# Kernel tuning notes

Hardware: AMD Instinct MI355X
Metric: run time of the kernel (lower is better)

The kernel has to match this reference:

```python
import jax, jax.numpy as jnp
import numpy as np

N_NODES = 100000
N_EDGES = 3200000


def setup_inputs() -> dict:
    key = jax.random.key(0)
    ks = jax.random.split(key, 12)
    x = jax.random.normal(ks[0], (N_NODES, 5), dtype=jnp.float32)
    edges = jax.random.randint(ks[1], (2, N_EDGES), 0, N_NODES)
    edge_attr = jax.random.normal(ks[2], (N_EDGES, 2), dtype=jnp.float32)
    detector_labels = jax.random.bernoulli(ks[3], 0.7, (N_NODES,))

    def init(k, shape, fan_in):
        return (jax.random.normal(k, shape, dtype=jnp.float32) / np.sqrt(fan_in)).astype(jnp.float32)

    W_gat = init(ks[4], (5, 16), 5)        # GATConv lin (shared src/dst)
    att_src = init(ks[5], (16,), 16)
    att_dst = init(ks[6], (16,), 16)
    W_edge = init(ks[7], (2, 16), 2)       # GATConv lin_edge
    att_edge = init(ks[8], (16,), 16)
    b_gat = jnp.zeros((16,), jnp.float32)
    W1 = init(ks[9], (34, 64), 34)
    b1 = jnp.zeros((64,), jnp.float32)
    W2 = init(ks[10], (64, 2), 64)
    b2 = jnp.zeros((2,), jnp.float32)
    return dict(x=x, edges=edges, edge_attr=edge_attr, detector_labels=detector_labels,
                W_gat=W_gat, att_src=att_src, att_dst=att_dst, W_edge=W_edge,
                att_edge=att_edge, b_gat=b_gat, W1=W1, b1=b1, W2=W2, b2=b2)


def reference(x, edges, edge_attr, detector_labels, W_gat, att_src, att_dst,
              W_edge, att_edge, b_gat, W1, b1, W2, b2):
    n_nodes = x.shape[0]
    src, dst = edges[0], edges[1]

    # --- GATConv(5 -> 16, heads=1, concat=False, edge_dim=2, no self loops) ---
    h = x @ W_gat                                        # [N, 16]
    a_src = h @ att_src                                  # [N]
    a_dst = h @ att_dst                                  # [N]
    a_edge = (edge_attr @ W_edge) @ att_edge             # [E]
    alpha = jax.nn.leaky_relu(a_src[src] + a_dst[dst] + a_edge, 0.2)
    # segmented softmax over incoming edges of each dst node
    seg_max = jax.ops.segment_max(alpha, dst, num_segments=n_nodes)
    ex = jnp.exp(alpha - seg_max[dst])
    denom = jax.ops.segment_sum(ex, dst, num_segments=n_nodes)
    a = ex / (denom[dst] + 1e-16)                        # [E]
    out = jax.ops.segment_sum(h[src] * a[:, None], dst, num_segments=n_nodes) + b_gat
    xh = jax.nn.relu(out)                                # [N, 16]

    # --- edge update: gather-concat-MLP ---
    feat = jnp.concatenate([xh[src], edge_attr, xh[dst]], axis=-1)   # [E, 34]
    ef = jax.nn.relu(feat @ W1 + b1) @ W2 + b2                       # [E, 2]

    # --- SplitSyndromes: keep edges whose both endpoints are detectors ---
    valid = detector_labels[src] & detector_labels[dst]
    idx = jnp.nonzero(valid)[0]        # eager (data-dependent size, not jitted)
    return edges[:, idx], jax.nn.sigmoid(ef[idx])
```

## Files before the change

### kernel.cpp

```cpp
#include <hip/hip_runtime.h>

#define NN 100000
#define NE 3200000
#define CH 8192
#define NCB ((NE + CH - 1) / CH)
#define ITER (CH / 256)
#define NBK ((NN + 63) >> 6)
#define CAP 2560

__global__ void kdetect(const unsigned char* __restrict__ lab8, int* __restrict__ flags) {
  __shared__ int tmp[256];
  int t = threadIdx.x;
  int s = 0;
  for (int i = t; i < 25000; i += 256) s += lab8[4 * i + 1];
  tmp[t] = s;
  __syncthreads();
  for (int d = 128; d > 0; d >>= 1) { if (t < d) tmp[t] += tmp[t + d]; __syncthreads(); }
  if (t == 0) flags[0] = (tmp[0] != 0) ? 1 : 0;
}

__global__ void klab(const void* __restrict__ lab, const int* __restrict__ flags,
                     int* __restrict__ labN) {
  int n = blockIdx.x * 256 + threadIdx.x;
  if (n >= NN) return;
  int v;
  if (flags[0]) v = ((const unsigned char*)lab)[n];
  else          v = ((const int*)lab)[n];
  labN[n] = (v != 0) ? 1 : 0;
}

__global__ void kc01(const float* __restrict__ We, const float* __restrict__ ae,
                     float* __restrict__ c01) {
  if (threadIdx.x == 0) {
    float c0 = 0.f, c1 = 0.f;
    for (int k = 0; k < 16; k++) { c0 += We[k] * ae[k]; c1 += We[16 + k] * ae[k]; }
    c01[0] = c0; c01[1] = c1;
  }
}

__global__ void knodeA(const float* __restrict__ x, const float* __restrict__ Wg,
                       const float* __restrict__ atts, const float* __restrict__ attd,
                       float* __restrict__ a_src, float* __restrict__ a_dst) {
  int n = blockIdx.x * 256 + threadIdx.x;
  if (n >= NN) return;
  float xi[5];
#pragma unroll
  for (int i = 0; i < 5; i++) xi[i] = x[n * 5 + i];
  float asum = 0.f, dsum = 0.f;
#pragma unroll
  for (int k = 0; k < 16; k++) {
    float acc = 0.f;
#pragma unroll
    for (int i = 0; i < 5; i++) acc += xi[i] * Wg[i * 16 + k];
    asum += acc * atts[k];
    dsum += acc * attd[k];
  }
  a_src[n] = asum; a_dst[n] = dsum;
}

__global__ __launch_bounds__(256) void khist(const int* __restrict__ src,
                                             const int* __restrict__ dst,
                                             const int* __restrict__ labN,
                                             int* __restrict__ blkcnt,
                                             int* __restrict__ cntc) {
  __shared__ int hist[NBK];
  __shared__ int vsum;
  int tid = threadIdx.x, b = blockIdx.x;
  for (int i = tid; i < NBK; i += 256) hist[i] = 0;
  if (tid == 0) vsum = 0;
  __syncthreads();
  int wsum = 0;
  for (int it = 0; it < ITER; ++it) {
    int e = b * CH + it * 256 + tid;
    int v = 0;
    if (e < NE) {
      int s = src[e], d = dst[e];
      atomicAdd(&hist[d >> 6], 1);
      v = labN[s] & labN[d];
    }
    unsigned long long m = __ballot(v != 0);
    wsum += __popcll(m);
  }
  if ((tid & 63) == 0) atomicAdd(&vsum, wsum);
  __syncthreads();
  for (int i = tid; i < NBK; i += 256) blkcnt[i * NCB + b] = hist[i];
  if (tid == 0) cntc[b] = vsum;
}

__global__ __launch_bounds__(256) void kscanb(int* __restrict__ blkcnt,
                                              int* __restrict__ total) {
  __shared__ int a[512];
  int row = blockIdx.x, t = threadIdx.x;
  int* p = blkcnt + row * NCB;
  int o0 = (t < NCB) ? p[t] : 0;
  int o1 = (t + 256 < NCB) ? p[t + 256] : 0;
  a[t] = o0; a[t + 256] = o1;
  __syncthreads();
  for (int d = 1; d < 512; d <<= 1) {
    int x0 = (t >= d) ? a[t - d] : 0;
    int x1 = (t + 256 >= d) ? a[t + 256 - d] : 0;
    __syncthreads();
    a[t] += x0; a[t + 256] += x1;
    __syncthreads();
  }
  if (t < NCB) p[t] = a[t] - o0;
  if (t + 256 < NCB) p[t + 256] = a[t + 256] - o1;
  if (t == 0) total[row] = a[NCB - 1];
}

__global__ void kscan(const int* __restrict__ cnt, int* __restrict__ off, int nb) {
  __shared__ int tmp[256];
  __shared__ int carry;
  int t = threadIdx.x;
  if (t == 0) carry = 0;
  __syncthreads();
  for (int base = 0; base < nb; base += 256) {
    int i = base + t;
    int v = (i < nb) ? cnt[i] : 0;
    tmp[t] = v;
    __syncthreads();
    for (int d = 1; d < 256; d <<= 1) {
      int add = (t >= d) ? tmp[t - d] : 0;
      __syncthreads();
      tmp[t] += add;
      __syncthreads();
    }
    if (i < nb) off[i] = carry + tmp[t] - v;
    __syncthreads();
    if (t == 0) carry += tmp[255];
    __syncthreads();
  }
  if (t == 0) off[nb] = carry;
}

__global__ __launch_bounds__(256) void kscat(
    const int* __restrict__ src, const int* __restrict__ dst,
    const float* __restrict__ eattr, const int* __restrict__ labN,
    const float* __restrict__ a_src, const float* __restrict__ a_dst,
    const float* __restrict__ c01, const int* __restrict__ bucket_base,
    const int* __restrict__ blkcnt, const int* __restrict__ offc,
    uint2* __restrict__ bins, float* __restrict__ out,
    float2* __restrict__ eat2, int NV) {
  __shared__ int cur[NBK];
  __shared__ int wc[4];
  __shared__ int lbase;
  int b = blockIdx.x, tid = threadIdx.x;
  for (int i = tid; i < NBK; i += 256) cur[i] = bucket_base[i] + blkcnt[i * NCB + b];
  if (tid == 0) lbase = offc[b];
  float c0 = c01[0], c1 = c01[1];
  __syncthreads();
  int lane = tid & 63, wid = tid >> 6;
  for (int it = 0; it < ITER; ++it) {
    int e = b * CH + it * 256 + tid;
    int v = 0, s = 0, d = 0;
    float2 ea;
    if (e < NE) {
      s = src[e]; d = dst[e];
      ea = ((const float2*)eattr)[e];
      float al = a_src[s] + a_dst[d] + ea.x * c0 + ea.y * c1;
      al = (al > 0.f) ? al : 0.2f * al;
      float exv = __expf(al);
      int pos = atomicAdd(&cur[d >> 6], 1);
      uint2 pl;
      pl.x = ((unsigned)s << 6) | (unsigned)(d & 63);
      pl.y = __float_as_uint(exv);
      bins[pos] = pl;
      v = labN[s] & labN[d];
    }
    unsigned long long m = __ballot(v != 0);
    if (lane == 0) wc[wid] = __popcll(m);
    __syncthreads();
    int pre = 0;
    for (int i = 0; i < wid; i++) pre += wc[i];
    pre += __popcll(m & ((1ull << lane) - 1ull));
    if (v) {
      int p = lbase + pre;
      if (p < NV) {
        out[p] = (float)s;
        out[NV + p] = (float)d;
        eat2[p] = ea;
      }
    }
    __syncthreads();
    if (tid == 0) lbase += wc[0] + wc[1] + wc[2] + wc[3];
  }
}

__global__ __launch_bounds__(512) void kagg(
    const uint2* __restrict__ bins, const int* __restrict__ bucket_base,
    const float* __restrict__ x, const float* __restrict__ Wg,
    const float* __restrict__ bg, float* __restrict__ xh) {
  __shared__ uint2 pay[CAP];
  __shared__ int cnt[64], inc[64], cur[64];
  __shared__ float sWg[80], sbg[16];
  int k = blockIdx.x, tid = threadIdx.x;
  if (tid < 80) sWg[tid] = Wg[tid];
  else if (tid < 96) sbg[tid - 80] = bg[tid - 80];
  int start = bucket_base[k], end = bucket_base[k + 1];
  int node0 = k << 6;
  int c = tid & 15, g = tid >> 4;
  __syncthreads();
  float w0 = sWg[c], w1 = sWg[16 + c], w2 = sWg[32 + c], w3 = sWg[48 + c], w4 = sWg[64 + c];
  float acc[2] = {0.f, 0.f}, den[2] = {0.f, 0.f};
  for (int cb = start; cb < end; cb += CAP) {
    int n = min(end - cb, CAP);
    if (tid < 64) cnt[tid] = 0;
    __syncthreads();
    uint2 st0, st1, st2, st3, st4;
    {
      int i;
      i = tid;          if (i < n) { st0 = bins[cb + i]; atomicAdd(&cnt[st0.x & 63], 1); }
      i = tid + 512;    if (i < n) { st1 = bins[cb + i]; atomicAdd(&cnt[st1.x & 63], 1); }
      i = tid + 1024;   if (i < n) { st2 = bins[cb + i]; atomicAdd(&cnt[st2.x & 63], 1); }
      i = tid + 1536;   if (i < n) { st3 = bins[cb + i]; atomicAdd(&cnt[st3.x & 63], 1); }
      i = tid + 2048;   if (i < n) { st4 = bins[cb + i]; atomicAdd(&cnt[st4.x & 63], 1); }
    }
    __syncthreads();
    if (tid < 64) inc[tid] = cnt[tid];
    __syncthreads();
    for (int d = 1; d < 64; d <<= 1) {
      int v = 0;
      if (tid >= d && tid < 64) v = inc[tid - d];
      __syncthreads();
      if (tid < 64) inc[tid] += v;
      __syncthreads();
    }
    if (tid < 64) cur[tid] = inc[tid] - cnt[tid];
    __syncthreads();
    {
      int i;
      i = tid;          if (i < n) pay[atomicAdd(&cur[st0.x & 63], 1)] = st0;
      i = tid + 512;    if (i < n) pay[atomicAdd(&cur[st1.x & 63], 1)] = st1;
      i = tid + 1024;   if (i < n) pay[atomicAdd(&cur[st2.x & 63], 1)] = st2;
      i = tid + 1536;   if (i < n) pay[atomicAdd(&cur[st3.x & 63], 1)] = st3;
      i = tid + 2048;   if (i < n) pay[atomicAdd(&cur[st4.x & 63], 1)] = st4;
    }
    __syncthreads();
#pragma unroll
    for (int p = 0; p < 2; ++p) {
      int nd = p * 32 + g;
      int re = inc[nd], rs = re - cnt[nd];
      float a = 0.f, ds = 0.f;
      for (int idx = rs; idx < re; ++idx) {
        uint2 pl = pay[idx];
        int s = (int)(pl.x >> 6);
        float exv = __uint_as_float(pl.y);
        const float* xp = x + s * 5;
        float h = xp[0] * w0 + xp[1] * w1 + xp[2] * w2 + xp[3] * w3 + xp[4] * w4;
        a += h * exv;
        ds += exv;
      }
      acc[p] += a; den[p] += ds;
    }
    __syncthreads();
  }
#pragma unroll
  for (int p = 0; p < 2; ++p) {
    int node = node0 + p * 32 + g;
    if (node < NN) {
      float dn = fmaxf(den[p], 1e-30f);
      float v = acc[p] / dn + sbg[c];
      xh[node * 16 + c] = (v > 0.f) ? v : 0.f;
    }
  }
}

__global__ __launch_bounds__(256) void kmlp(
    const float2* __restrict__ eat2, const float* __restrict__ xh,
    const float* __restrict__ W1, const float* __restrict__ b1,
    const float* __restrict__ W2, const float* __restrict__ b2,
    float* __restrict__ out, int NV) {
  __shared__ __align__(16) float sW1[34 * 64];
  __shared__ __align__(16) float sb1[64];
  __shared__ float sW2[128];
  __shared__ float sb2[2];
  for (int i = threadIdx.x; i < 34 * 64; i += 256) sW1[i] = W1[i];
  if (threadIdx.x < 64) sb1[threadIdx.x] = b1[threadIdx.x];
  if (threadIdx.x < 128) sW2[threadIdx.x] = W2[threadIdx.x];
  if (threadIdx.x < 2) sb2[threadIdx.x] = b2[threadIdx.x];
  __syncthreads();
  int p = blockIdx.x * 256 + threadIdx.x;
  if (p >= NV) return;
  int s = (int)out[p];
  int d = (int)out[NV + p];
  float feat[34];
  const float4* xs = (const float4*)(xh + s * 16);
  const float4* xd = (const float4*)(xh + d * 16);
#pragma unroll
  for (int q = 0; q < 4; q++) {
    float4 t = xs[q];
    feat[q * 4 + 0] = t.x; feat[q * 4 + 1] = t.y; feat[q * 4 + 2] = t.z; feat[q * 4 + 3] = t.w;
  }
  {
    float2 ea = eat2[p];
    feat[16] = ea.x; feat[17] = ea.y;
  }
#pragma unroll
  for (int q = 0; q < 4; q++) {
    float4 t = xd[q];
    feat[18 + q * 4 + 0] = t.x; feat[18 + q * 4 + 1] = t.y;
    feat[18 + q * 4 + 2] = t.z; feat[18 + q * 4 + 3] = t.w;
  }
  float o0 = sb2[0], o1 = sb2[1];
  for (int jb = 0; jb < 64; jb += 4) {
    float4 acc = *(const float4*)(sb1 + jb);
#pragma unroll
    for (int i = 0; i < 34; i++) {
      float4 w = *(const float4*)(sW1 + i * 64 + jb);
      float f = feat[i];
      acc.x += f * w.x; acc.y += f * w.y; acc.z += f * w.z; acc.w += f * w.w;
    }
    acc.x = fmaxf(acc.x, 0.f); acc.y = fmaxf(acc.y, 0.f);
    acc.z = fmaxf(acc.z, 0.f); acc.w = fmaxf(acc.w, 0.f);
    o0 += acc.x * sW2[(jb + 0) * 2]     + acc.y * sW2[(jb + 1) * 2]
        + acc.z * sW2[(jb + 2) * 2]     + acc.w * sW2[(jb + 3) * 2];
    o1 += acc.x * sW2[(jb + 0) * 2 + 1] + acc.y * sW2[(jb + 1) * 2 + 1]
        + acc.z * sW2[(jb + 2) * 2 + 1] + acc.w * sW2[(jb + 3) * 2 + 1];
  }
  out[2 * NV + 2 * p + 0] = 1.f / (1.f + __expf(-o0));
  out[2 * NV + 2 * p + 1] = 1.f / (1.f + __expf(-o1));
}

static inline size_t al64(size_t v) { return (v + 63) & ~(size_t)63; }

extern "C" void kernel_launch(void* const* d_in, const int* in_sizes, int n_in,
                              void* d_out, int out_size, void* d_ws, size_t ws_size,
                              hipStream_t stream) {
  const float* x     = (const float*)d_in[0];
  const int*   edges = (const int*)d_in[1];
  const float* eattr = (const float*)d_in[2];
  const void*  labels= d_in[3];
  const float* Wg    = (const float*)d_in[4];
  const float* atts  = (const float*)d_in[5];
  const float* attd  = (const float*)d_in[6];
  const float* We    = (const float*)d_in[7];
  const float* atte  = (const float*)d_in[8];
  const float* bg    = (const float*)d_in[9];
  const float* W1    = (const float*)d_in[10];
  const float* b1    = (const float*)d_in[11];
  const float* W2    = (const float*)d_in[12];
  const float* b2    = (const float*)d_in[13];
  float* out = (float*)d_out;
  const int NV = out_size / 4;
  const int* src = edges;
  const int* dst = edges + NE;

  char* w = (char*)d_ws;
  float* xh    = (float*)w;   w += al64((size_t)NN * 64);
  uint2* bins  = (uint2*)w;   w += al64((size_t)NE * 8);
  float2* eat2 = (float2*)w;  w += al64((size_t)NV * 8);
  float* a_src = (float*)w;   w += al64((size_t)NN * 4);
  float* a_dst = (float*)w;   w += al64((size_t)NN * 4);
  int* labN    = (int*)w;     w += al64((size_t)NN * 4);
  int* blkcnt  = (int*)w;     w += al64((size_t)NBK * NCB * 4);
  int* total   = (int*)w;     w += al64((size_t)NBK * 4);
  int* bb      = (int*)w;     w += al64((size_t)(NBK + 1) * 4);
  int* cntc    = (int*)w;     w += al64((size_t)NCB * 4);
  int* offc    = (int*)w;     w += al64((size_t)(NCB + 1) * 4);
  float* c01   = (float*)w;   w += 64;
  int* flags   = (int*)w;     w += 64;

  kdetect<<<1, 256, 0, stream>>>((const unsigned char*)labels, flags);
  klab<<<(NN + 255) / 256, 256, 0, stream>>>(labels, flags, labN);
  kc01<<<1, 64, 0, stream>>>(We, atte, c01);
  knodeA<<<(NN + 255) / 256, 256, 0, stream>>>(x, Wg, atts, attd, a_src, a_dst);
  khist<<<NCB, 256, 0, stream>>>(src, dst, labN, blkcnt, cntc);
  kscanb<<<NBK, 256, 0, stream>>>(blkcnt, total);
  kscan<<<1, 256, 0, stream>>>(total, bb, NBK);
  kscan<<<1, 256, 0, stream>>>(cntc, offc, NCB);
  kscat<<<NCB, 256, 0, stream>>>(src, dst, eattr, labN, a_src, a_dst, c01, bb, blkcnt,
                                 offc, bins, out, eat2, NV);
  kagg<<<NBK, 512, 0, stream>>>(bins, bb, x, Wg, bg, xh);
  if (NV > 0)
    kmlp<<<(NV + 255) / 256, 256, 0, stream>>>(eat2, xh, W1, b1, W2, b2, out, NV);
}
```

Baseline: 342.4 us.

## Precompute per-node first-layer MLP projections and gather them per edge

The first MLP layer is split by linearity. A new kernel computes, per node, u = xh·W1[src rows] + b1 and v = xh·W1[dst rows]. The edge kernel then only gathers u[src] and v[dst], adds the two-column edge-attribute term, and applies ReLU and the second layer. This removes the 34x64 per-edge matmul and its LDS weight reads. In exchange, each edge gathers 512 bytes of random node data instead of 128, adds an extra kernel launch, and reuses the bins buffer for u.

Result: slower. 414.4 us (+21.0%).

```diff
diff --git a/kernel.cpp b/kernel.cpp
--- a/kernel.cpp
+++ b/kernel.cpp
@@ -265,57 +265,79 @@
   }
 }
 
-__global__ __launch_bounds__(256) void kmlp(
-    const float2* __restrict__ eat2, const float* __restrict__ xh,
-    const float* __restrict__ W1, const float* __restrict__ b1,
+__global__ __launch_bounds__(256) void kprep(
+    const float* __restrict__ xh, const float* __restrict__ W1,
+    const float* __restrict__ b1, float* __restrict__ u, float* __restrict__ v) {
+  __shared__ float sW1[34 * 64];
+  __shared__ float sb1[64];
+  for (int i = threadIdx.x; i < 34 * 64; i += 256) sW1[i] = W1[i];
+  if (threadIdx.x < 64) sb1[threadIdx.x] = b1[threadIdx.x];
+  __syncthreads();
+  int t = threadIdx.x;
+  int node = blockIdx.x * 16 + (t >> 4);
+  if (node >= NN) return;
+  int jq = (t & 15) * 4;
+  float xf[16];
+  const float4* xp = (const float4*)(xh + node * 16);
+#pragma unroll
+  for (int q = 0; q < 4; q++) {
+    float4 tv = xp[q];
+    xf[q * 4 + 0] = tv.x; xf[q * 4 + 1] = tv.y;
+    xf[q * 4 + 2] = tv.z; xf[q * 4 + 3] = tv.w;
+  }
+  float uu[4], vv[4];
+#pragma unroll
+  for (int j = 0; j < 4; j++) { uu[j] = sb1[jq + j]; vv[j] = 0.f; }
+#pragma unroll
+  for (int i = 0; i < 16; i++) {
+    float f = xf[i];
+    const float* wu = sW1 + i * 64 + jq;
+    const float* wv = sW1 + (18 + i) * 64 + jq;
+#pragma unroll
+    for (int j = 0; j < 4; j++) {
+      uu[j] += f * wu[j];
+      vv[j] += f * wv[j];
+    }
+  }
+  *(float4*)(u + (size_t)node * 64 + jq) = make_float4(uu[0], uu[1], uu[2], uu[3]);
+  *(float4*)(v + (size_t)node * 64 + jq) = make_float4(vv[0], vv[1], vv[2], vv[3]);
+}
+
+__global__ __launch_bounds__(256) void kmlp2(
+    const float2* __restrict__ eat2, const float* __restrict__ u,
+    const float* __restrict__ v, const float* __restrict__ W1,
     const float* __restrict__ W2, const float* __restrict__ b2,
     float* __restrict__ out, int NV) {
-  __shared__ __align__(16) float sW1[34 * 64];
-  __shared__ __align__(16) float sb1[64];
+  __shared__ float sE[128];
   __shared__ float sW2[128];
   __shared__ float sb2[2];
-  for (int i = threadIdx.x; i < 34 * 64; i += 256) sW1[i] = W1[i];
-  if (threadIdx.x < 64) sb1[threadIdx.x] = b1[threadIdx.x];
-  if (threadIdx.x < 128) sW2[threadIdx.x] = W2[threadIdx.x];
+  if (threadIdx.x < 128) sE[threadIdx.x] = W1[16 * 64 + threadIdx.x];
+  else sW2[threadIdx.x - 128] = W2[threadIdx.x - 128];
   if (threadIdx.x < 2) sb2[threadIdx.x] = b2[threadIdx.x];
   __syncthreads();
   int p = blockIdx.x * 256 + threadIdx.x;
   if (p >= NV) return;
   int s = (int)out[p];
   int d = (int)out[NV + p];
-  float feat[34];
-  const float4* xs = (const float4*)(xh + s * 16);
-  const float4* xd = (const float4*)(xh + d * 16);
-#pragma unroll
-  for (int q = 0; q < 4; q++) {
-    float4 t = xs[q];
-    feat[q * 4 + 0] = t.x; feat[q * 4 + 1] = t.y; feat[q * 4 + 2] = t.z; feat[q * 4 + 3] = t.w;
-  }
-  {
-    float2 ea = eat2[p];
-    feat[16] = ea.x; feat[17] = ea.y;
-  }
-#pragma unroll
-  for (int q = 0; q < 4; q++) {
-    float4 t = xd[q];
-    feat[18 + q * 4 + 0] = t.x; feat[18 + q * 4 + 1] = t.y;
-    feat[18 + q * 4 + 2] = t.z; feat[18 + q * 4 + 3] = t.w;
-  }
+  float2 ea = eat2[p];
+  const float4* up = (const float4*)(u + (size_t)s * 64);
+  const float4* vp = (const float4*)(v + (size_t)d * 64);
   float o0 = sb2[0], o1 = sb2[1];
-  for (int jb = 0; jb < 64; jb += 4) {
-    float4 acc = *(const float4*)(sb1 + jb);
-#pragma unroll
-    for (int i = 0; i < 34; i++) {
-      float4 w = *(const float4*)(sW1 + i * 64 + jb);
-      float f = feat[i];
-      acc.x += f * w.x; acc.y += f * w.y; acc.z += f * w.z; acc.w += f * w.w;
-    }
-    acc.x = fmaxf(acc.x, 0.f); acc.y = fmaxf(acc.y, 0.f);
-    acc.z = fmaxf(acc.z, 0.f); acc.w = fmaxf(acc.w, 0.f);
-    o0 += acc.x * sW2[(jb + 0) * 2]     + acc.y * sW2[(jb + 1) * 2]
-        + acc.z * sW2[(jb + 2) * 2]     + acc.w * sW2[(jb + 3) * 2];
-    o1 += acc.x * sW2[(jb + 0) * 2 + 1] + acc.y * sW2[(jb + 1) * 2 + 1]
-        + acc.z * sW2[(jb + 2) * 2 + 1] + acc.w * sW2[(jb + 3) * 2 + 1];
+#pragma unroll
+  for (int q = 0; q < 16; q++) {
+    float4 a = up[q];
+    float4 b = vp[q];
+    const float* e0 = sE + q * 4;
+    const float* e1 = sE + 64 + q * 4;
+    float h0 = a.x + b.x + ea.x * e0[0] + ea.y * e1[0];
+    float h1 = a.y + b.y + ea.x * e0[1] + ea.y * e1[1];
+    float h2 = a.z + b.z + ea.x * e0[2] + ea.y * e1[2];
+    float h3 = a.w + b.w + ea.x * e0[3] + ea.y * e1[3];
+    h0 = fmaxf(h0, 0.f); h1 = fmaxf(h1, 0.f);
+    h2 = fmaxf(h2, 0.f); h3 = fmaxf(h3, 0.f);
+    const float* w2p = sW2 + q * 8;
+    o0 += h0 * w2p[0] + h1 * w2p[2] + h2 * w2p[4] + h3 * w2p[6];
+    o1 += h0 * w2p[1] + h1 * w2p[3] + h2 * w2p[5] + h3 * w2p[7];
   }
   out[2 * NV + 2 * p + 0] = 1.f / (1.f + __expf(-o0));
   out[2 * NV + 2 * p + 1] = 1.f / (1.f + __expf(-o1));
@@ -359,6 +381,8 @@
   int* offc    = (int*)w;     w += al64((size_t)(NCB + 1) * 4);
   float* c01   = (float*)w;   w += 64;
   int* flags   = (int*)w;     w += 64;
+  float* uvec  = (float*)bins;
+  float* vvec  = (float*)w;   w += al64((size_t)NN * 256);
 
   kdetect<<<1, 256, 0, stream>>>((const unsigned char*)labels, flags);
   klab<<<(NN + 255) / 256, 256, 0, stream>>>(labels, flags, labN);
@@ -371,6 +395,7 @@
   kscat<<<NCB, 256, 0, stream>>>(src, dst, eattr, labN, a_src, a_dst, c01, bb, blkcnt,
                                  offc, bins, out, eat2, NV);
   kagg<<<NBK, 512, 0, stream>>>(bins, bb, x, Wg, bg, xh);
+  kprep<<<(NN + 15) / 16, 256, 0, stream>>>(xh, W1, b1, uvec, vvec);
   if (NV > 0)
-    kmlp<<<(NV + 255) / 256, 256, 0, stream>>>(eat2, xh, W1, b1, W2, b2, out, NV);
-}
+    kmlp2<<<(NV + 255) / 256, 256, 0, stream>>>(eat2, uvec, vvec, W1, W2, b2, out, NV);
+}
```

## Run edge MLP first layer on MFMA with split-bf16 emulated fp32

Applied to the files above, without the earlier changes.

Rewrites the edge MLP kernel so the 32-input part of the first layer (the xh[src] and xh[dst] features) runs as 16x16x32 bf16 MFMA. Weights and activations are split into high and low bf16 halves and three products are summed to approximate fp32 accuracy. The edge_attr terms, bias, ReLU and second layer stay in scalar code and are reduced with wave shuffles. The launch becomes a fixed 2048-block grid-stride loop with weights held in registers instead of shared memory. This aims to cut the per-edge scalar FMA cost, at the price of small precision loss and extra shuffle work.

Measured after the change: 286.3 us. -16.4%, faster.

```diff
diff --git a/kernel.cpp b/kernel.cpp
--- a/kernel.cpp
+++ b/kernel.cpp
@@ -7,6 +7,11 @@
 #define ITER (CH / 256)
 #define NBK ((NN + 63) >> 6)
 #define CAP 2560
+
+typedef __attribute__((ext_vector_type(8))) __bf16 bf16x8;
+typedef __attribute__((ext_vector_type(4))) float f32x4;
+
+union BF8 { unsigned short u[8]; bf16x8 v; };
 
 __global__ void kdetect(const unsigned char* __restrict__ lab8, int* __restrict__ flags) {
   __shared__ int tmp[256];
@@ -270,55 +275,105 @@
     const float* __restrict__ W1, const float* __restrict__ b1,
     const float* __restrict__ W2, const float* __restrict__ b2,
     float* __restrict__ out, int NV) {
-  __shared__ __align__(16) float sW1[34 * 64];
-  __shared__ __align__(16) float sb1[64];
-  __shared__ float sW2[128];
-  __shared__ float sb2[2];
-  for (int i = threadIdx.x; i < 34 * 64; i += 256) sW1[i] = W1[i];
-  if (threadIdx.x < 64) sb1[threadIdx.x] = b1[threadIdx.x];
-  if (threadIdx.x < 128) sW2[threadIdx.x] = W2[threadIdx.x];
-  if (threadIdx.x < 2) sb2[threadIdx.x] = b2[threadIdx.x];
-  __syncthreads();
-  int p = blockIdx.x * 256 + threadIdx.x;
-  if (p >= NV) return;
-  int s = (int)out[p];
-  int d = (int)out[NV + p];
-  float feat[34];
-  const float4* xs = (const float4*)(xh + s * 16);
-  const float4* xd = (const float4*)(xh + d * 16);
-#pragma unroll
-  for (int q = 0; q < 4; q++) {
-    float4 t = xs[q];
-    feat[q * 4 + 0] = t.x; feat[q * 4 + 1] = t.y; feat[q * 4 + 2] = t.z; feat[q * 4 + 3] = t.w;
-  }
-  {
-    float2 ea = eat2[p];
-    feat[16] = ea.x; feat[17] = ea.y;
-  }
-#pragma unroll
-  for (int q = 0; q < 4; q++) {
-    float4 t = xd[q];
-    feat[18 + q * 4 + 0] = t.x; feat[18 + q * 4 + 1] = t.y;
-    feat[18 + q * 4 + 2] = t.z; feat[18 + q * 4 + 3] = t.w;
-  }
-  float o0 = sb2[0], o1 = sb2[1];
-  for (int jb = 0; jb < 64; jb += 4) {
-    float4 acc = *(const float4*)(sb1 + jb);
-#pragma unroll
-    for (int i = 0; i < 34; i++) {
-      float4 w = *(const float4*)(sW1 + i * 64 + jb);
-      float f = feat[i];
-      acc.x += f * w.x; acc.y += f * w.y; acc.z += f * w.z; acc.w += f * w.w;
-    }
-    acc.x = fmaxf(acc.x, 0.f); acc.y = fmaxf(acc.y, 0.f);
-    acc.z = fmaxf(acc.z, 0.f); acc.w = fmaxf(acc.w, 0.f);
-    o0 += acc.x * sW2[(jb + 0) * 2]     + acc.y * sW2[(jb + 1) * 2]
-        + acc.z * sW2[(jb + 2) * 2]     + acc.w * sW2[(jb + 3) * 2];
-    o1 += acc.x * sW2[(jb + 0) * 2 + 1] + acc.y * sW2[(jb + 1) * 2 + 1]
-        + acc.z * sW2[(jb + 2) * 2 + 1] + acc.w * sW2[(jb + 3) * 2 + 1];
-  }
-  out[2 * NV + 2 * p + 0] = 1.f / (1.f + __expf(-o0));
-  out[2 * NV + 2 * p + 1] = 1.f / (1.f + __expf(-o1));
+  int tid = threadIdx.x;
+  int lane = tid & 63, wid = tid >> 6;
+  int lo4 = lane & 15, q = lane >> 4;
+
+  BF8 bh[4], bl[4];
+#pragma unroll
+  for (int ct = 0; ct < 4; ct++) {
+    int col = ct * 16 + lo4;
+#pragma unroll
+    for (int i = 0; i < 8; i++) {
+      int k = q * 8 + i;
+      int r = (k < 16) ? k : (k + 2);
+      float w = W1[r * 64 + col];
+      unsigned u = __float_as_uint(w);
+      float rem = w - __uint_as_float(u & 0xffff0000u);
+      bh[ct].u[i] = (unsigned short)(u >> 16);
+      bl[ct].u[i] = (unsigned short)(__float_as_uint(rem) >> 16);
+    }
+  }
+  float b1v[4], w16v[4], w17v[4], w2a[4], w2b[4];
+#pragma unroll
+  for (int ct = 0; ct < 4; ct++) {
+    int j = ct * 16 + lo4;
+    b1v[ct] = b1[j];
+    w16v[ct] = W1[16 * 64 + j];
+    w17v[ct] = W1[17 * 64 + j];
+    w2a[ct] = W2[j * 2 + 0];
+    w2b[ct] = W2[j * 2 + 1];
+  }
+  float bias20 = b2[0], bias21 = b2[1];
+
+  int nwaves = gridDim.x * 4;
+  int ntiles = (NV + 15) >> 4;
+  for (int tb = blockIdx.x * 4 + wid; tb < ntiles; tb += nwaves) {
+    int base = tb * 16;
+    BF8 ah, al;
+    {
+      int p = base + lo4;
+      float vals[8] = {0.f, 0.f, 0.f, 0.f, 0.f, 0.f, 0.f, 0.f};
+      if (p < NV) {
+        int node = (int)out[((q < 2) ? 0 : NV) + p];
+        const float4* xp = (const float4*)(xh + node * 16 + (q & 1) * 8);
+        float4 f0 = xp[0], f1 = xp[1];
+        vals[0] = f0.x; vals[1] = f0.y; vals[2] = f0.z; vals[3] = f0.w;
+        vals[4] = f1.x; vals[5] = f1.y; vals[6] = f1.z; vals[7] = f1.w;
+      }
+#pragma unroll
+      for (int i = 0; i < 8; i++) {
+        unsigned u = __float_as_uint(vals[i]);
+        float rem = vals[i] - __uint_as_float(u & 0xffff0000u);
+        ah.u[i] = (unsigned short)(u >> 16);
+        al.u[i] = (unsigned short)(__float_as_uint(rem) >> 16);
+      }
+    }
+    f32x4 acc[4];
+#pragma unroll
+    for (int ct = 0; ct < 4; ct++) {
+      f32x4 z = {0.f, 0.f, 0.f, 0.f};
+      z = __builtin_amdgcn_mfma_f32_16x16x32_bf16(ah.v, bh[ct].v, z, 0, 0, 0);
+      z = __builtin_amdgcn_mfma_f32_16x16x32_bf16(ah.v, bl[ct].v, z, 0, 0, 0);
+      z = __builtin_amdgcn_mfma_f32_16x16x32_bf16(al.v, bh[ct].v, z, 0, 0, 0);
+      acc[ct] = z;
+    }
+    float o0[4], o1[4];
+#pragma unroll
+    for (int reg = 0; reg < 4; reg++) {
+      int pr = base + q * 4 + reg;
+      float2 ea = make_float2(0.f, 0.f);
+      if (pr < NV) ea = eat2[pr];
+      float s0 = 0.f, s1 = 0.f;
+#pragma unroll
+      for (int ct = 0; ct < 4; ct++) {
+        float h = acc[ct][reg] + b1v[ct] + ea.x * w16v[ct] + ea.y * w17v[ct];
+        h = fmaxf(h, 0.f);
+        s0 += h * w2a[ct];
+        s1 += h * w2b[ct];
+      }
+      o0[reg] = s0; o1[reg] = s1;
+    }
+#pragma unroll
+    for (int m = 1; m < 16; m <<= 1) {
+#pragma unroll
+      for (int reg = 0; reg < 4; reg++) {
+        o0[reg] += __shfl_xor(o0[reg], m, 64);
+        o1[reg] += __shfl_xor(o1[reg], m, 64);
+      }
+    }
+    if (lo4 == 0) {
+#pragma unroll
+      for (int reg = 0; reg < 4; reg++) {
+        int pr = base + q * 4 + reg;
+        if (pr < NV) {
+          float v0 = bias20 + o0[reg], v1 = bias21 + o1[reg];
+          ((float2*)(out + 2 * (size_t)NV))[pr] = make_float2(
+              1.f / (1.f + __expf(-v0)), 1.f / (1.f + __expf(-v1)));
+        }
+      }
+    }
+  }
 }
 
 static inline size_t al64(size_t v) { return (v + 63) & ~(size_t)63; }
@@ -372,5 +427,5 @@
                                  offc, bins, out, eat2, NV);
   kagg<<<NBK, 512, 0, stream>>>(bins, bb, x, Wg, bg, xh);
   if (NV > 0)
-    kmlp<<<(NV + 255) / 256, 256, 0, stream>>>(eat2, xh, W1, b1, W2, b2, out, NV);
-}
+    kmlp<<<2048, 256, 0, stream>>>(eat2, xh, W1, b1, W2, b2, out, NV);
+}
```
